# Kernel tuning notes

Hardware: AMD Instinct MI355X
Metric: run time of the kernel (lower is better)

## Reference

```python
import jax, jax.numpy as jnp
import numpy as np

K_PROPOSALS = 16  # Marsaglia-Tsang acceptance rate > 0.95 for alpha > 1/3; P(all 16 rejected) < 1e-20

B, D_IN, H, L = 32768, 1024, 512, 64


def _glorot(key, shape):
    fan_in, fan_out = shape
    return jax.random.normal(key, shape, jnp.float32) * jnp.sqrt(2.0 / (fan_in + fan_out))


def setup_inputs() -> dict:
    key = jax.random.key(0)
    ks = jax.random.split(key, 4)
    return {
        "x": jax.random.normal(ks[0], (B, D_IN), jnp.float32),
        "W0": _glorot(ks[1], (D_IN, H)),
        "b0": jnp.zeros((H,), jnp.float32),
        "W1": _glorot(ks[2], (H, H)),
        "b1": jnp.zeros((H,), jnp.float32),
        "Wl": _glorot(ks[3], (H, L)),
        "bl": jnp.zeros((L,), jnp.float32),
    }


def _marsaglia_tsang_sample(alpha):
    """Vectorized Marsaglia-Tsang gamma(alpha, 1) rejection sampler.
    Draws K_PROPOSALS candidates per element and selects the first accepted one
    (equivalent to the original per-element while-loop, flattened for SIMD)."""
    d = alpha - 1.0 / 3.0                     # [B, L]
    c = 1.0 / jnp.sqrt(9.0 * d)               # [B, L]
    kz, ku = jax.random.split(jax.random.key(1))
    z = jax.random.normal(kz, (K_PROPOSALS,) + alpha.shape, alpha.dtype)   # [K, B, L]
    u = jax.random.uniform(ku, (K_PROPOSALS,) + alpha.shape, alpha.dtype,
                           minval=1e-7, maxval=1.0)                        # [K, B, L]
    v = (1.0 + c * z) ** 3                    # [K, B, L]
    pos = v > 0.0                             # equivalent to z > -1/c (= b1)
    safe_v = jnp.where(pos, v, 1.0)
    # accept iff z > b1 AND log(u) <= b2 (negation of the resampling condition)
    b2 = 0.5 * jnp.square(z) + d - d * safe_v + d * jnp.log(safe_v)
    accept = pos & (jnp.log(u) < b2)          # [K, B, L]
    first = jnp.argmax(accept, axis=0)        # index of first accepted proposal
    samples = d * safe_v                      # [K, B, L]
    return jnp.take_along_axis(samples, first[None], axis=0)[0]  # [B, L]


def reference(x, W0, b0, W1, b1, Wl, bl):
    # dense encoder: two ReLU hidden layers + linear latent head producing alpha
    h = jax.nn.relu(x @ W0 + b0)
    h = jax.nn.relu(h @ W1 + b1)
    # softplus + 0.5 keeps alpha > 1/3 so d > 0 (required by Marsaglia-Tsang)
    alpha = jax.nn.softplus(h @ Wl + bl) + 0.5
    sample = _marsaglia_tsang_sample(alpha)
    return alpha, sample
```

## Files before the change

kernel.cpp:

```cpp
#include <hip/hip_runtime.h>
#include <cstdint>
#include <cstddef>

typedef __attribute__((ext_vector_type(8))) short short8;
typedef __attribute__((ext_vector_type(4))) float floatx4;

constexpr int MDIM = 32768;
constexpr int DIN  = 1024;
constexpr int HDIM = 512;
constexpr int LDIM = 64;
constexpr uint32_t BL = (uint32_t)MDIM * (uint32_t)LDIM;

__host__ __device__ __forceinline__ void tf2x32(uint32_t k0, uint32_t k1,
                                                uint32_t x0, uint32_t x1,
                                                uint32_t& o0, uint32_t& o1) {
  const uint32_t k2 = k0 ^ k1 ^ 0x1BD11BDAu;
  x0 += k0; x1 += k1;
#define TFR(r) { x0 += x1; x1 = (x1 << (r)) | (x1 >> (32 - (r))); x1 ^= x0; }
  TFR(13) TFR(15) TFR(26) TFR(6)
  x0 += k1; x1 += k2 + 1u;
  TFR(17) TFR(29) TFR(16) TFR(24)
  x0 += k2; x1 += k0 + 2u;
  TFR(13) TFR(15) TFR(26) TFR(6)
  x0 += k0; x1 += k1 + 3u;
  TFR(17) TFR(29) TFR(16) TFR(24)
  x0 += k1; x1 += k2 + 4u;
  TFR(13) TFR(15) TFR(26) TFR(6)
  x0 += k2; x1 += k0 + 5u;
#undef TFR
  o0 = x0; o1 = x1;
}

__device__ __forceinline__ uint32_t tf_bits(uint32_t k0, uint32_t k1, uint32_t j) {
  uint32_t o0, o1;
  tf2x32(k0, k1, 0u, j, o0, o1);
  return o0 ^ o1;
}

__device__ __forceinline__ float b2f(unsigned short s) {
  return __uint_as_float((uint32_t)s << 16);
}
__device__ __forceinline__ unsigned short f2b(float f) {
  uint32_t u = __float_as_uint(f);
  u += 0x7fffu + ((u >> 16) & 1u);
  return (unsigned short)(u >> 16);
}
__device__ __forceinline__ void split3(float x, unsigned short& h,
                                       unsigned short& l, unsigned short& l2) {
  h = f2b(x);
  const float r = __fsub_rn(x, b2f(h));
  l = f2b(r);
  const float r2 = __fsub_rn(r, b2f(l));
  l2 = f2b(r2);
}

__device__ __forceinline__ float erfinv_f32(float x) {
  const float xx = __fmul_rn(x, x);
  float w = -log1pf(-xx);
  float p;
  if (w < 5.0f) {
    w = __fadd_rn(w, -2.5f);
    p = 2.81022636e-08f;
    p = __fadd_rn(__fmul_rn(p, w), 3.43273939e-07f);
    p = __fadd_rn(__fmul_rn(p, w), -3.5233877e-06f);
    p = __fadd_rn(__fmul_rn(p, w), -4.39150654e-06f);
    p = __fadd_rn(__fmul_rn(p, w), 0.00021858087f);
    p = __fadd_rn(__fmul_rn(p, w), -0.00125372503f);
    p = __fadd_rn(__fmul_rn(p, w), -0.00417768164f);
    p = __fadd_rn(__fmul_rn(p, w), 0.246640727f);
    p = __fadd_rn(__fmul_rn(p, w), 1.50140941f);
  } else {
    w = __fadd_rn(sqrtf(w), -3.0f);
    p = -0.000200214257f;
    p = __fadd_rn(__fmul_rn(p, w), 0.000100950558f);
    p = __fadd_rn(__fmul_rn(p, w), 0.00134934322f);
    p = __fadd_rn(__fmul_rn(p, w), -0.00367342844f);
    p = __fadd_rn(__fmul_rn(p, w), 0.00573950773f);
    p = __fadd_rn(__fmul_rn(p, w), -0.0076224613f);
    p = __fadd_rn(__fmul_rn(p, w), 0.00943887047f);
    p = __fadd_rn(__fmul_rn(p, w), 1.00167406f);
    p = __fadd_rn(__fmul_rn(p, w), 2.83297682f);
  }
  return __fmul_rn(p, x);
}

#define LO_N  (-0x1.fffffep-1f)
#define DIFF_N (2.0f)
#define SQRT2_F ((float)1.4142135623730951)
#define DIFF_U (0x1.fffffcp-1f)
#define MINV_U (1e-7f)
#define THIRD_F ((float)(1.0 / 3.0))

__device__ float gamma_sample(float alpha, uint32_t e,
                              uint32_t kz0, uint32_t kz1,
                              uint32_t ku0, uint32_t ku1) {
  const float d = __fsub_rn(alpha, THIRD_F);
  const float c = __fdiv_rn(1.0f, sqrtf(__fmul_rn(9.0f, d)));
  float samp0 = 0.0f;
#pragma unroll 1
  for (int k = 0; k < 16; ++k) {
    const uint32_t j = (uint32_t)k * BL + e;
    const uint32_t zb = tf_bits(kz0, kz1, j);
    const uint32_t ub = tf_bits(ku0, ku1, j);
    const float fz = __fsub_rn(__uint_as_float((zb >> 9) | 0x3f800000u), 1.0f);
    float un = __fadd_rn(__fmul_rn(fz, DIFF_N), LO_N);
    un = fmaxf(un, LO_N);
    const float z = __fmul_rn(SQRT2_F, erfinv_f32(un));
    const float fu = __fsub_rn(__uint_as_float((ub >> 9) | 0x3f800000u), 1.0f);
    float uu = __fadd_rn(__fmul_rn(fu, DIFF_U), MINV_U);
    uu = fmaxf(uu, MINV_U);
    const float t1 = __fadd_rn(1.0f, __fmul_rn(c, z));
    const float v = __fmul_rn(t1, __fmul_rn(t1, t1));
    const bool pos = (v > 0.0f);
    const float sv = pos ? v : 1.0f;
    const float b2 = __fadd_rn(
        __fsub_rn(__fadd_rn(__fmul_rn(0.5f, __fmul_rn(z, z)), d),
                  __fmul_rn(d, sv)),
        __fmul_rn(d, logf(sv)));
    const float lu = logf(uu);
    const float s = __fmul_rn(d, sv);
    if (k == 0) samp0 = s;
    if (pos && (lu < b2)) return s;
  }
  return samp0;
}

__global__ __launch_bounds__(256) void split_transpose(
    const float* __restrict__ W, unsigned short* __restrict__ D, int K, int N) {
  __shared__ unsigned short th[32][33], tl[32][33], tl2[32][33];
  const int t = threadIdx.x;
  const int nb = N / 32;
  const int k0 = (blockIdx.x / nb) * 32, n0 = (blockIdx.x % nb) * 32;
#pragma unroll
  for (int i = 0; i < 4; ++i) {
    const int e = i * 256 + t;
    const int kk = e >> 5, nn = e & 31;
    const float x = W[(size_t)(k0 + kk) * N + (n0 + nn)];
    split3(x, th[kk][nn], tl[kk][nn], tl2[kk][nn]);
  }
  __syncthreads();
  const size_t PL = (size_t)N * K;
#pragma unroll
  for (int i = 0; i < 4; ++i) {
    const int e = i * 256 + t;
    const int nn = e >> 5, kk = e & 31;
    const size_t o = (size_t)(n0 + nn) * K + (k0 + kk);
    D[o] = th[kk][nn];
    D[PL + o] = tl[kk][nn];
    D[2 * PL + o] = tl2[kk][nn];
  }
}

template <int K>
__global__ __launch_bounds__(256) void gemm_split_mfma(
    const float* __restrict__ A, const unsigned short* __restrict__ BT,
    const float* __restrict__ bias, float* __restrict__ C) {
  constexpr int N = 512;
  constexpr size_t PL = (size_t)N * K;
  __shared__ unsigned short As[3][128 * 32];
  __shared__ unsigned short Bs[3][128 * 32];
  const int t = threadIdx.x;
  const int lane = t & 63, w = t >> 6;
  const int wm = w >> 1, wn = w & 1;
  const int ln = lane & 15, kq = lane >> 4;
  const int bid = blockIdx.y * gridDim.x + blockIdx.x;
  const int L = (bid & 7) * 128 + (bid >> 3);
  const int bm = (L >> 2) * 128, bn = (L & 3) * 128;
  const int rq = kq ^ ((ln >> 1) & 3);
  const int kcs = ((lane & 3) ^ ((lane >> 3) & 3)) * 8;

  floatx4 acc[4][4];
#pragma unroll
  for (int i = 0; i < 4; ++i)
#pragma unroll
    for (int j = 0; j < 4; ++j) acc[i][j] = (floatx4)0.0f;

  for (int k0 = 0; k0 < K; k0 += 32) {
#pragma unroll
    for (int p = 0; p < 3; ++p)
#pragma unroll
      for (int i = 0; i < 2; ++i) {
        const int e = w * 1024 + i * 512 + lane * 8;
        const int n = e >> 5;
        const unsigned short* g = BT + p * PL + (size_t)(bn + n) * K + (k0 + kcs);
        __builtin_amdgcn_global_load_lds(
            (const __attribute__((address_space(1))) unsigned int*)g,
            (__attribute__((address_space(3))) unsigned int*)&Bs[p][w * 1024 + i * 512],
            16, 0, 0);
      }
#pragma unroll
    for (int it = 0; it < 4; ++it) {
      const int e4 = (it * 256 + t) * 4;
      const int m = e4 >> 5, kc = e4 & 31;
      const float4 q = *reinterpret_cast<const float4*>(
          &A[(size_t)(bm + m) * K + (k0 + kc)]);
      ushort4 h, l, l2;
      split3(q.x, h.x, l.x, l2.x);
      split3(q.y, h.y, l.y, l2.y);
      split3(q.z, h.z, l.z, l2.z);
      split3(q.w, h.w, l.w, l2.w);
      const int si = m * 32 + (((kc >> 3) ^ ((m >> 1) & 3)) << 3) + (kc & 7);
      *reinterpret_cast<ushort4*>(&As[0][si]) = h;
      *reinterpret_cast<ushort4*>(&As[1][si]) = l;
      *reinterpret_cast<ushort4*>(&As[2][si]) = l2;
    }
    __syncthreads();
    short8 af[3][4], bf[3][4];
#pragma unroll
    for (int mi = 0; mi < 4; ++mi)
#pragma unroll
      for (int p = 0; p < 3; ++p)
        af[p][mi] = *reinterpret_cast<const short8*>(
            &As[p][(wm * 64 + mi * 16 + ln) * 32 + rq * 8]);
#pragma unroll
    for (int ni = 0; ni < 4; ++ni)
#pragma unroll
      for (int p = 0; p < 3; ++p)
        bf[p][ni] = *reinterpret_cast<const short8*>(
            &Bs[p][(wn * 64 + ni * 16 + ln) * 32 + rq * 8]);
#pragma unroll
    for (int mi = 0; mi < 4; ++mi)
#pragma unroll
      for (int ni = 0; ni < 4; ++ni) {
        floatx4 a = acc[mi][ni];
        a = __builtin_amdgcn_mfma_f32_16x16x32_bf16(af[0][mi], bf[0][ni], a, 0, 0, 0);
        a = __builtin_amdgcn_mfma_f32_16x16x32_bf16(af[0][mi], bf[1][ni], a, 0, 0, 0);
        a = __builtin_amdgcn_mfma_f32_16x16x32_bf16(af[1][mi], bf[0][ni], a, 0, 0, 0);
        a = __builtin_amdgcn_mfma_f32_16x16x32_bf16(af[1][mi], bf[1][ni], a, 0, 0, 0);
        a = __builtin_amdgcn_mfma_f32_16x16x32_bf16(af[0][mi], bf[2][ni], a, 0, 0, 0);
        a = __builtin_amdgcn_mfma_f32_16x16x32_bf16(af[2][mi], bf[0][ni], a, 0, 0, 0);
        acc[mi][ni] = a;
      }
    __syncthreads();
  }
#pragma unroll
  for (int ni = 0; ni < 4; ++ni) {
    const int n = bn + wn * 64 + ni * 16 + ln;
    const float bb = bias[n];
#pragma unroll
    for (int mi = 0; mi < 4; ++mi)
#pragma unroll
      for (int r = 0; r < 4; ++r) {
        const int m = bm + wm * 64 + mi * 16 + kq * 4 + r;
        C[(size_t)m * N + n] = fmaxf(__fadd_rn(acc[mi][ni][r], bb), 0.0f);
      }
  }
}

__global__ __launch_bounds__(256) void gemm3_alpha(
    const float* __restrict__ A, const unsigned short* __restrict__ BT,
    const float* __restrict__ bl, float* __restrict__ out) {
  constexpr int K = 512, N = 64;
  constexpr size_t PL = (size_t)N * K;
  __shared__ unsigned short As[3][64 * 32];
  __shared__ unsigned short Bs[3][64 * 32];
  const int t = threadIdx.x;
  const int lane = t & 63, w = t >> 6;
  const int ln = lane & 15, kq = lane >> 4;
  const int bm = blockIdx.x * 64;
  const int rq = kq ^ ((ln >> 1) & 3);
  const int kcs = ((lane & 3) ^ ((lane >> 3) & 3)) * 8;

  floatx4 acc[4];
#pragma unroll
  for (int j = 0; j < 4; ++j) acc[j] = (floatx4)0.0f;

  for (int k0 = 0; k0 < K; k0 += 32) {
#pragma unroll
    for (int p = 0; p < 3; ++p) {
      const int n = w * 16 + (lane >> 2);
      const unsigned short* g = BT + p * PL + (size_t)n * K + (k0 + kcs);
      __builtin_amdgcn_global_load_lds(
          (const __attribute__((address_space(1))) unsigned int*)g,
          (__attribute__((address_space(3))) unsigned int*)&Bs[p][w * 512],
          16, 0, 0);
    }
#pragma unroll
    for (int it = 0; it < 2; ++it) {
      const int e4 = (it * 256 + t) * 4;
      const int m = e4 >> 5, kc = e4 & 31;
      const float4 q = *reinterpret_cast<const float4*>(
          &A[(size_t)(bm + m) * K + (k0 + kc)]);
      ushort4 h, l, l2;
      split3(q.x, h.x, l.x, l2.x);
      split3(q.y, h.y, l.y, l2.y);
      split3(q.z, h.z, l.z, l2.z);
      split3(q.w, h.w, l.w, l2.w);
      const int si = m * 32 + (((kc >> 3) ^ ((m >> 1) & 3)) << 3) + (kc & 7);
      *reinterpret_cast<ushort4*>(&As[0][si]) = h;
      *reinterpret_cast<ushort4*>(&As[1][si]) = l;
      *reinterpret_cast<ushort4*>(&As[2][si]) = l2;
    }
    __syncthreads();
    short8 af[3];
#pragma unroll
    for (int p = 0; p < 3; ++p)
      af[p] = *reinterpret_cast<const short8*>(
          &As[p][(w * 16 + ln) * 32 + rq * 8]);
#pragma unroll
    for (int ni = 0; ni < 4; ++ni) {
      const short8 b0 = *reinterpret_cast<const short8*>(
          &Bs[0][(ni * 16 + ln) * 32 + rq * 8]);
      const short8 b1 = *reinterpret_cast<const short8*>(
          &Bs[1][(ni * 16 + ln) * 32 + rq * 8]);
      const short8 b2 = *reinterpret_cast<const short8*>(
          &Bs[2][(ni * 16 + ln) * 32 + rq * 8]);
      floatx4 a = acc[ni];
      a = __builtin_amdgcn_mfma_f32_16x16x32_bf16(af[0], b0, a, 0, 0, 0);
      a = __builtin_amdgcn_mfma_f32_16x16x32_bf16(af[0], b1, a, 0, 0, 0);
      a = __builtin_amdgcn_mfma_f32_16x16x32_bf16(af[1], b0, a, 0, 0, 0);
      a = __builtin_amdgcn_mfma_f32_16x16x32_bf16(af[1], b1, a, 0, 0, 0);
      a = __builtin_amdgcn_mfma_f32_16x16x32_bf16(af[0], b2, a, 0, 0, 0);
      a = __builtin_amdgcn_mfma_f32_16x16x32_bf16(af[2], b0, a, 0, 0, 0);
      acc[ni] = a;
    }
    __syncthreads();
  }
#pragma unroll
  for (int ni = 0; ni < 4; ++ni) {
    const int n = ni * 16 + ln;
    const float bb = bl[n];
#pragma unroll
    for (int r = 0; r < 4; ++r) {
      const int m = bm + w * 16 + kq * 4 + r;
      const float x = __fadd_rn(acc[ni][r], bb);
      const float sp = __fadd_rn(fmaxf(x, 0.0f), log1pf(expf(-fabsf(x))));
      out[(size_t)m * 64 + n] = __fadd_rn(sp, 0.5f);
    }
  }
}

__global__ __launch_bounds__(256) void gamma_kernel(
    const float* __restrict__ alpha, float* __restrict__ smp,
    uint32_t kz0, uint32_t kz1, uint32_t ku0, uint32_t ku1) {
  const uint32_t i4 = ((uint32_t)blockIdx.x * 256u + (uint32_t)threadIdx.x) * 4u;
  const float4 a = *reinterpret_cast<const float4*>(&alpha[i4]);
  float4 s;
  s.x = gamma_sample(a.x, i4 + 0u, kz0, kz1, ku0, ku1);
  s.y = gamma_sample(a.y, i4 + 1u, kz0, kz1, ku0, ku1);
  s.z = gamma_sample(a.z, i4 + 2u, kz0, kz1, ku0, ku1);
  s.w = gamma_sample(a.w, i4 + 3u, kz0, kz1, ku0, ku1);
  *reinterpret_cast<float4*>(&smp[i4]) = s;
}

extern "C" void kernel_launch(void* const* d_in, const int* in_sizes, int n_in,
                              void* d_out, int out_size, void* d_ws, size_t ws_size,
                              hipStream_t stream) {
  (void)in_sizes; (void)n_in; (void)out_size; (void)ws_size;
  const float* x  = (const float*)d_in[0];
  const float* W0 = (const float*)d_in[1];
  const float* b0 = (const float*)d_in[2];
  const float* W1 = (const float*)d_in[3];
  const float* b1 = (const float*)d_in[4];
  const float* Wl = (const float*)d_in[5];
  const float* bl = (const float*)d_in[6];
  float* h1 = (float*)d_ws;
  float* h2 = h1 + (size_t)MDIM * HDIM;
  float* out = (float*)d_out;

  unsigned short* W0T = (unsigned short*)out;
  unsigned short* W1T = (unsigned short*)(out + BL);
  unsigned short* WlT = (unsigned short*)d_ws;

  uint32_t kz0, kz1, ku0, ku1;
  tf2x32(0u, 1u, 0u, 0u, kz0, kz1);
  tf2x32(0u, 1u, 0u, 1u, ku0, ku1);

  split_transpose<<<dim3((DIN / 32) * (HDIM / 32)), 256, 0, stream>>>(
      W0, W0T, DIN, HDIM);
  split_transpose<<<dim3((HDIM / 32) * (HDIM / 32)), 256, 0, stream>>>(
      W1, W1T, HDIM, HDIM);

  dim3 g12(HDIM / 128, MDIM / 128);
  gemm_split_mfma<DIN><<<g12, 256, 0, stream>>>(x, W0T, b0, h1);
  gemm_split_mfma<HDIM><<<g12, 256, 0, stream>>>(h1, W1T, b1, h2);

  split_transpose<<<dim3((HDIM / 32) * (LDIM / 32)), 256, 0, stream>>>(
      Wl, WlT, HDIM, LDIM);

  gemm3_alpha<<<dim3(MDIM / 64), 256, 0, stream>>>(h2, WlT, bl, out);

  gamma_kernel<<<dim3(BL / 1024), 256, 0, stream>>>(out, out + BL,
                                                    kz0, kz1, ku0, ku1);
}
```

Measured before the change: 516.0 us.

## Use 512-thread blocks with 256-row tiles for split-bf16 GEMMs

The two hidden-layer GEMMs move from 256-thread blocks with 128x128 tiles to 512-thread blocks with 256x128 tiles, so each B tile is reused across twice as many rows. The swizzled block-ID remapping is dropped. The alpha GEMM also runs with 512 threads, using a 2D warp split so each wave handles 16 rows by 32 columns. The aim is less B-operand traffic per output and more waves per block. The costs are a larger LDS footprint, tighter register limits from launch_bounds(512,4), and the loss of the L2-friendly block ordering.

```diff
diff --git a/kernel.cpp b/kernel.cpp
--- a/kernel.cpp
+++ b/kernel.cpp
@@ -152,20 +152,18 @@
 }
 
 template <int K>
-__global__ __launch_bounds__(256) void gemm_split_mfma(
+__device__ __forceinline__ void gemm_body(
     const float* __restrict__ A, const unsigned short* __restrict__ BT,
     const float* __restrict__ bias, float* __restrict__ C) {
   constexpr int N = 512;
   constexpr size_t PL = (size_t)N * K;
-  __shared__ unsigned short As[3][128 * 32];
+  __shared__ unsigned short As[3][256 * 32];
   __shared__ unsigned short Bs[3][128 * 32];
   const int t = threadIdx.x;
   const int lane = t & 63, w = t >> 6;
   const int wm = w >> 1, wn = w & 1;
   const int ln = lane & 15, kq = lane >> 4;
-  const int bid = blockIdx.y * gridDim.x + blockIdx.x;
-  const int L = (bid & 7) * 128 + (bid >> 3);
-  const int bm = (L >> 2) * 128, bn = (L & 3) * 128;
+  const int bm = blockIdx.y * 256, bn = blockIdx.x * 128;
   const int rq = kq ^ ((ln >> 1) & 3);
   const int kcs = ((lane & 3) ^ ((lane >> 3) & 3)) * 8;
 
@@ -177,20 +175,17 @@
 
   for (int k0 = 0; k0 < K; k0 += 32) {
 #pragma unroll
-    for (int p = 0; p < 3; ++p)
-#pragma unroll
-      for (int i = 0; i < 2; ++i) {
-        const int e = w * 1024 + i * 512 + lane * 8;
-        const int n = e >> 5;
-        const unsigned short* g = BT + p * PL + (size_t)(bn + n) * K + (k0 + kcs);
-        __builtin_amdgcn_global_load_lds(
-            (const __attribute__((address_space(1))) unsigned int*)g,
-            (__attribute__((address_space(3))) unsigned int*)&Bs[p][w * 1024 + i * 512],
-            16, 0, 0);
-      }
+    for (int p = 0; p < 3; ++p) {
+      const int n = w * 16 + (lane >> 2);
+      const unsigned short* g = BT + p * PL + (size_t)(bn + n) * K + (k0 + kcs);
+      __builtin_amdgcn_global_load_lds(
+          (const __attribute__((address_space(1))) unsigned int*)g,
+          (__attribute__((address_space(3))) unsigned int*)&Bs[p][w * 512],
+          16, 0, 0);
+    }
 #pragma unroll
     for (int it = 0; it < 4; ++it) {
-      const int e4 = (it * 256 + t) * 4;
+      const int e4 = (it * 512 + t) * 4;
       const int m = e4 >> 5, kc = e4 & 31;
       const float4 q = *reinterpret_cast<const float4*>(
           &A[(size_t)(bm + m) * K + (k0 + kc)]);
@@ -247,7 +242,18 @@
   }
 }
 
-__global__ __launch_bounds__(256) void gemm3_alpha(
+__global__ __launch_bounds__(512, 4) void gemm1_k1024(
+    const float* __restrict__ A, const unsigned short* __restrict__ BT,
+    const float* __restrict__ bias, float* __restrict__ C) {
+  gemm_body<DIN>(A, BT, bias, C);
+}
+__global__ __launch_bounds__(512, 4) void gemm2_k512(
+    const float* __restrict__ A, const unsigned short* __restrict__ BT,
+    const float* __restrict__ bias, float* __restrict__ C) {
+  gemm_body<HDIM>(A, BT, bias, C);
+}
+
+__global__ __launch_bounds__(512, 4) void gemm3_alpha(
     const float* __restrict__ A, const unsigned short* __restrict__ BT,
     const float* __restrict__ bl, float* __restrict__ out) {
   constexpr int K = 512, N = 64;
@@ -256,74 +262,74 @@
   __shared__ unsigned short Bs[3][64 * 32];
   const int t = threadIdx.x;
   const int lane = t & 63, w = t >> 6;
+  const int wm = w >> 1, wn = w & 1;
   const int ln = lane & 15, kq = lane >> 4;
   const int bm = blockIdx.x * 64;
   const int rq = kq ^ ((ln >> 1) & 3);
   const int kcs = ((lane & 3) ^ ((lane >> 3) & 3)) * 8;
-
-  floatx4 acc[4];
-#pragma unroll
-  for (int j = 0; j < 4; ++j) acc[j] = (floatx4)0.0f;
+  const int arow = t >> 3, acol = (t * 4) & 31;
+  const int swz = ((((acol >> 3) ^ ((arow >> 1) & 3)) << 3) | (acol & 7));
+
+  floatx4 acc[2];
+  acc[0] = (floatx4)0.0f;
+  acc[1] = (floatx4)0.0f;
 
   for (int k0 = 0; k0 < K; k0 += 32) {
-#pragma unroll
-    for (int p = 0; p < 3; ++p) {
-      const int n = w * 16 + (lane >> 2);
+    for (int s2 = w; s2 < 12; s2 += 8) {
+      const int p = s2 >> 2, half = s2 & 3;
+      const int n = half * 16 + (lane >> 2);
       const unsigned short* g = BT + p * PL + (size_t)n * K + (k0 + kcs);
       __builtin_amdgcn_global_load_lds(
           (const __attribute__((address_space(1))) unsigned int*)g,
-          (__attribute__((address_space(3))) unsigned int*)&Bs[p][w * 512],
+          (__attribute__((address_space(3))) unsigned int*)&Bs[p][half * 512],
           16, 0, 0);
     }
-#pragma unroll
-    for (int it = 0; it < 2; ++it) {
-      const int e4 = (it * 256 + t) * 4;
-      const int m = e4 >> 5, kc = e4 & 31;
+    {
       const float4 q = *reinterpret_cast<const float4*>(
-          &A[(size_t)(bm + m) * K + (k0 + kc)]);
+          &A[(size_t)(bm + arow) * K + (k0 + acol)]);
       ushort4 h, l, l2;
       split3(q.x, h.x, l.x, l2.x);
       split3(q.y, h.y, l.y, l2.y);
       split3(q.z, h.z, l.z, l2.z);
       split3(q.w, h.w, l.w, l2.w);
-      const int si = m * 32 + (((kc >> 3) ^ ((m >> 1) & 3)) << 3) + (kc & 7);
+      const int si = arow * 32 + swz;
       *reinterpret_cast<ushort4*>(&As[0][si]) = h;
       *reinterpret_cast<ushort4*>(&As[1][si]) = l;
       *reinterpret_cast<ushort4*>(&As[2][si]) = l2;
     }
     __syncthreads();
-    short8 af[3];
+    short8 af[3], bf[3][2];
 #pragma unroll
     for (int p = 0; p < 3; ++p)
       af[p] = *reinterpret_cast<const short8*>(
-          &As[p][(w * 16 + ln) * 32 + rq * 8]);
-#pragma unroll
-    for (int ni = 0; ni < 4; ++ni) {
-      const short8 b0 = *reinterpret_cast<const short8*>(
-          &Bs[0][(ni * 16 + ln) * 32 + rq * 8]);
-      const short8 b1 = *reinterpret_cast<const short8*>(
-          &Bs[1][(ni * 16 + ln) * 32 + rq * 8]);
-      const short8 b2 = *reinterpret_cast<const short8*>(
-          &Bs[2][(ni * 16 + ln) * 32 + rq * 8]);
-      floatx4 a = acc[ni];
-      a = __builtin_amdgcn_mfma_f32_16x16x32_bf16(af[0], b0, a, 0, 0, 0);
-      a = __builtin_amdgcn_mfma_f32_16x16x32_bf16(af[0], b1, a, 0, 0, 0);
-      a = __builtin_amdgcn_mfma_f32_16x16x32_bf16(af[1], b0, a, 0, 0, 0);
-      a = __builtin_amdgcn_mfma_f32_16x16x32_bf16(af[1], b1, a, 0, 0, 0);
-      a = __builtin_amdgcn_mfma_f32_16x16x32_bf16(af[0], b2, a, 0, 0, 0);
-      a = __builtin_amdgcn_mfma_f32_16x16x32_bf16(af[2], b0, a, 0, 0, 0);
-      acc[ni] = a;
+          &As[p][(wm * 16 + ln) * 32 + rq * 8]);
+#pragma unroll
+    for (int j = 0; j < 2; ++j)
+#pragma unroll
+      for (int p = 0; p < 3; ++p)
+        bf[p][j] = *reinterpret_cast<const short8*>(
+            &Bs[p][(wn * 32 + j * 16 + ln) * 32 + rq * 8]);
+#pragma unroll
+    for (int j = 0; j < 2; ++j) {
+      floatx4 a = acc[j];
+      a = __builtin_amdgcn_mfma_f32_16x16x32_bf16(af[0], bf[0][j], a, 0, 0, 0);
+      a = __builtin_amdgcn_mfma_f32_16x16x32_bf16(af[0], bf[1][j], a, 0, 0, 0);
+      a = __builtin_amdgcn_mfma_f32_16x16x32_bf16(af[1], bf[0][j], a, 0, 0, 0);
+      a = __builtin_amdgcn_mfma_f32_16x16x32_bf16(af[1], bf[1][j], a, 0, 0, 0);
+      a = __builtin_amdgcn_mfma_f32_16x16x32_bf16(af[0], bf[2][j], a, 0, 0, 0);
+      a = __builtin_amdgcn_mfma_f32_16x16x32_bf16(af[2], bf[0][j], a, 0, 0, 0);
+      acc[j] = a;
     }
     __syncthreads();
   }
 #pragma unroll
-  for (int ni = 0; ni < 4; ++ni) {
-    const int n = ni * 16 + ln;
+  for (int j = 0; j < 2; ++j) {
+    const int n = wn * 32 + j * 16 + ln;
     const float bb = bl[n];
 #pragma unroll
     for (int r = 0; r < 4; ++r) {
-      const int m = bm + w * 16 + kq * 4 + r;
-      const float x = __fadd_rn(acc[ni][r], bb);
+      const int m = bm + wm * 16 + kq * 4 + r;
+      const float x = __fadd_rn(acc[j][r], bb);
       const float sp = __fadd_rn(fmaxf(x, 0.0f), log1pf(expf(-fabsf(x))));
       out[(size_t)m * 64 + n] = __fadd_rn(sp, 0.5f);
     }
@@ -371,14 +377,14 @@
   split_transpose<<<dim3((HDIM / 32) * (HDIM / 32)), 256, 0, stream>>>(
       W1, W1T, HDIM, HDIM);
 
-  dim3 g12(HDIM / 128, MDIM / 128);
-  gemm_split_mfma<DIN><<<g12, 256, 0, stream>>>(x, W0T, b0, h1);
-  gemm_split_mfma<HDIM><<<g12, 256, 0, stream>>>(h1, W1T, b1, h2);
+  dim3 g12(HDIM / 128, MDIM / 256);
+  gemm1_k1024<<<g12, 512, 0, stream>>>(x, W0T, b0, h1);
+  gemm2_k512<<<g12, 512, 0, stream>>>(h1, W1T, b1, h2);
 
   split_transpose<<<dim3((HDIM / 32) * (LDIM / 32)), 256, 0, stream>>>(
       Wl, WlT, HDIM, LDIM);
 
-  gemm3_alpha<<<dim3(MDIM / 64), 256, 0, stream>>>(h2, WlT, bl, out);
+  gemm3_alpha<<<dim3(MDIM / 64), 512, 0, stream>>>(h2, WlT, bl, out);
 
   gamma_kernel<<<dim3(BL / 1024), 256, 0, stream>>>(out, out + BL,
                                                     kz0, kz1, ku0, ku1);
```

Result: slower. 538.6 us (+4.4%).

## Switch split-bf16 GEMMs to 32x32x16 MFMA and split first GEMM launch

Applied to the files above, without the earlier changes.

Replaces the 16x16x32 bf16 MFMA tiling in the two hidden-layer GEMMs with 32x32x16 MFMA, using 2x2 floatx16 accumulators per wave. Each k-step is split into two 16-wide sub-steps with matching swizzled LDS reads. The goal is fewer LDS fragment loads per FLOP and higher MFMA throughput. It also drops the block-index remapping swizzle and launches the first GEMM as two half-M kernels, which may change L2 locality and adds a launch.

```diff
diff --git a/kernel.cpp b/kernel.cpp
--- a/kernel.cpp
+++ b/kernel.cpp
@@ -4,6 +4,7 @@
 
 typedef __attribute__((ext_vector_type(8))) short short8;
 typedef __attribute__((ext_vector_type(4))) float floatx4;
+typedef __attribute__((ext_vector_type(16))) float floatx16;
 
 constexpr int MDIM = 32768;
 constexpr int DIN  = 1024;
@@ -152,9 +153,9 @@
 }
 
 template <int K>
-__global__ __launch_bounds__(256) void gemm_split_mfma(
+__device__ __forceinline__ void gemm_body32(
     const float* __restrict__ A, const unsigned short* __restrict__ BT,
-    const float* __restrict__ bias, float* __restrict__ C) {
+    const float* __restrict__ bias, float* __restrict__ C, const int bm) {
   constexpr int N = 512;
   constexpr size_t PL = (size_t)N * K;
   __shared__ unsigned short As[3][128 * 32];
@@ -162,18 +163,17 @@
   const int t = threadIdx.x;
   const int lane = t & 63, w = t >> 6;
   const int wm = w >> 1, wn = w & 1;
-  const int ln = lane & 15, kq = lane >> 4;
-  const int bid = blockIdx.y * gridDim.x + blockIdx.x;
-  const int L = (bid & 7) * 128 + (bid >> 3);
-  const int bm = (L >> 2) * 128, bn = (L & 3) * 128;
-  const int rq = kq ^ ((ln >> 1) & 3);
+  const int l31 = lane & 31, l5 = lane >> 5;
+  const int bn = blockIdx.x * 128;
   const int kcs = ((lane & 3) ^ ((lane >> 3) & 3)) * 8;
 
-  floatx4 acc[4][4];
-#pragma unroll
-  for (int i = 0; i < 4; ++i)
-#pragma unroll
-    for (int j = 0; j < 4; ++j) acc[i][j] = (floatx4)0.0f;
+  floatx16 acc[2][2];
+#pragma unroll
+  for (int i = 0; i < 2; ++i)
+#pragma unroll
+    for (int j = 0; j < 2; ++j)
+#pragma unroll
+      for (int q = 0; q < 16; ++q) acc[i][j][q] = 0.0f;
 
   for (int k0 = 0; k0 < K; k0 += 32) {
 #pragma unroll
@@ -205,46 +205,70 @@
       *reinterpret_cast<ushort4*>(&As[2][si]) = l2;
     }
     __syncthreads();
-    short8 af[3][4], bf[3][4];
-#pragma unroll
-    for (int mi = 0; mi < 4; ++mi)
-#pragma unroll
-      for (int p = 0; p < 3; ++p)
-        af[p][mi] = *reinterpret_cast<const short8*>(
-            &As[p][(wm * 64 + mi * 16 + ln) * 32 + rq * 8]);
-#pragma unroll
-    for (int ni = 0; ni < 4; ++ni)
-#pragma unroll
-      for (int p = 0; p < 3; ++p)
-        bf[p][ni] = *reinterpret_cast<const short8*>(
-            &Bs[p][(wn * 64 + ni * 16 + ln) * 32 + rq * 8]);
-#pragma unroll
-    for (int mi = 0; mi < 4; ++mi)
-#pragma unroll
-      for (int ni = 0; ni < 4; ++ni) {
-        floatx4 a = acc[mi][ni];
-        a = __builtin_amdgcn_mfma_f32_16x16x32_bf16(af[0][mi], bf[0][ni], a, 0, 0, 0);
-        a = __builtin_amdgcn_mfma_f32_16x16x32_bf16(af[0][mi], bf[1][ni], a, 0, 0, 0);
-        a = __builtin_amdgcn_mfma_f32_16x16x32_bf16(af[1][mi], bf[0][ni], a, 0, 0, 0);
-        a = __builtin_amdgcn_mfma_f32_16x16x32_bf16(af[1][mi], bf[1][ni], a, 0, 0, 0);
-        a = __builtin_amdgcn_mfma_f32_16x16x32_bf16(af[0][mi], bf[2][ni], a, 0, 0, 0);
-        a = __builtin_amdgcn_mfma_f32_16x16x32_bf16(af[2][mi], bf[0][ni], a, 0, 0, 0);
-        acc[mi][ni] = a;
+#pragma unroll
+    for (int ks = 0; ks < 2; ++ks) {
+      const int g = ks * 2 + l5;
+      short8 af[3][2], bf[3][2];
+#pragma unroll
+      for (int mi = 0; mi < 2; ++mi)
+#pragma unroll
+        for (int p = 0; p < 3; ++p) {
+          const int row = wm * 64 + mi * 32 + l31;
+          af[p][mi] = *reinterpret_cast<const short8*>(
+              &As[p][row * 32 + ((g ^ ((row >> 1) & 3)) << 3)]);
+        }
+#pragma unroll
+      for (int ni = 0; ni < 2; ++ni)
+#pragma unroll
+        for (int p = 0; p < 3; ++p) {
+          const int row = wn * 64 + ni * 32 + l31;
+          bf[p][ni] = *reinterpret_cast<const short8*>(
+              &Bs[p][row * 32 + ((g ^ ((row >> 1) & 3)) << 3)]);
+        }
+#pragma unroll
+      for (int mi = 0; mi < 2; ++mi)
+#pragma unroll
+        for (int ni = 0; ni < 2; ++ni) {
+          floatx16 a = acc[mi][ni];
+          a = __builtin_amdgcn_mfma_f32_32x32x16_bf16(af[0][mi], bf[0][ni], a, 0, 0, 0);
+          a = __builtin_amdgcn_mfma_f32_32x32x16_bf16(af[0][mi], bf[1][ni], a, 0, 0, 0);
+          a = __builtin_amdgcn_mfma_f32_32x32x16_bf16(af[1][mi], bf[0][ni], a, 0, 0, 0);
+          a = __builtin_amdgcn_mfma_f32_32x32x16_bf16(af[1][mi], bf[1][ni], a, 0, 0, 0);
+          a = __builtin_amdgcn_mfma_f32_32x32x16_bf16(af[0][mi], bf[2][ni], a, 0, 0, 0);
+          a = __builtin_amdgcn_mfma_f32_32x32x16_bf16(af[2][mi], bf[0][ni], a, 0, 0, 0);
+          acc[mi][ni] = a;
+        }
+    }
+    __syncthreads();
+  }
+#pragma unroll
+  for (int ni = 0; ni < 2; ++ni) {
+    const int col = bn + wn * 64 + ni * 32 + l31;
+    const float bb = bias[col];
+#pragma unroll
+    for (int mi = 0; mi < 2; ++mi)
+#pragma unroll
+      for (int r = 0; r < 16; ++r) {
+        const int row = bm + wm * 64 + mi * 32 + (r & 3) + 8 * (r >> 2) + 4 * l5;
+        C[(size_t)row * N + col] = fmaxf(__fadd_rn(acc[mi][ni][r], bb), 0.0f);
       }
-    __syncthreads();
-  }
-#pragma unroll
-  for (int ni = 0; ni < 4; ++ni) {
-    const int n = bn + wn * 64 + ni * 16 + ln;
-    const float bb = bias[n];
-#pragma unroll
-    for (int mi = 0; mi < 4; ++mi)
-#pragma unroll
-      for (int r = 0; r < 4; ++r) {
-        const int m = bm + wm * 64 + mi * 16 + kq * 4 + r;
-        C[(size_t)m * N + n] = fmaxf(__fadd_rn(acc[mi][ni][r], bb), 0.0f);
-      }
-  }
+  }
+}
+
+__global__ __launch_bounds__(256) void gemm1a(
+    const float* __restrict__ A, const unsigned short* __restrict__ BT,
+    const float* __restrict__ bias, float* __restrict__ C) {
+  gemm_body32<DIN>(A, BT, bias, C, blockIdx.y * 128);
+}
+__global__ __launch_bounds__(256) void gemm1b(
+    const float* __restrict__ A, const unsigned short* __restrict__ BT,
+    const float* __restrict__ bias, float* __restrict__ C) {
+  gemm_body32<DIN>(A, BT, bias, C, MDIM / 2 + blockIdx.y * 128);
+}
+__global__ __launch_bounds__(256) void gemm2_k512(
+    const float* __restrict__ A, const unsigned short* __restrict__ BT,
+    const float* __restrict__ bias, float* __restrict__ C) {
+  gemm_body32<HDIM>(A, BT, bias, C, blockIdx.y * 128);
 }
 
 __global__ __launch_bounds__(256) void gemm3_alpha(
@@ -371,9 +395,9 @@
   split_transpose<<<dim3((HDIM / 32) * (HDIM / 32)), 256, 0, stream>>>(
       W1, W1T, HDIM, HDIM);
 
-  dim3 g12(HDIM / 128, MDIM / 128);
-  gemm_split_mfma<DIN><<<g12, 256, 0, stream>>>(x, W0T, b0, h1);
-  gemm_split_mfma<HDIM><<<g12, 256, 0, stream>>>(h1, W1T, b1, h2);
+  gemm1a<<<dim3(HDIM / 128, MDIM / 256), 256, 0, stream>>>(x, W0T, b0, h1);
+  gemm1b<<<dim3(HDIM / 128, MDIM / 256), 256, 0, stream>>>(x, W0T, b0, h1);
+  gemm2_k512<<<dim3(HDIM / 128, MDIM / 128), 256, 0, stream>>>(h1, W1T, b1, h2);
 
   split_transpose<<<dim3((HDIM / 32) * (LDIM / 32)), 256, 0, stream>>>(
       Wl, WlT, HDIM, LDIM);
```

After: 546.8 us. +6.0%, slower.

## Split GEMM launches into row chunks and use one element per gamma thread

Applied to the files above, without the earlier changes.

Splits the first two GEMMs into several smaller launches over row ranges (3 for layer 1, 2 for layer 2), each with a plain blockIdx.x column mapping in place of the swizzled tile ordering. The gamma kernel now processes one element per thread instead of four with float4 loads. The intent is probably to change wave scheduling and tail behaviour and to raise parallelism in the divergent sampler. In exchange it drops the L2-friendly tile swizzle, adds launch overhead and loses vectorized memory access.

```diff
diff --git a/kernel.cpp b/kernel.cpp
--- a/kernel.cpp
+++ b/kernel.cpp
@@ -152,9 +152,9 @@
 }
 
 template <int K>
-__global__ __launch_bounds__(256) void gemm_split_mfma(
-    const float* __restrict__ A, const unsigned short* __restrict__ BT,
-    const float* __restrict__ bias, float* __restrict__ C) {
+__device__ __forceinline__ void gemm_body16(
+    const float* __restrict__ A, const unsigned short* __restrict__ BT,
+    const float* __restrict__ bias, float* __restrict__ C, const int bm) {
   constexpr int N = 512;
   constexpr size_t PL = (size_t)N * K;
   __shared__ unsigned short As[3][128 * 32];
@@ -163,9 +163,7 @@
   const int lane = t & 63, w = t >> 6;
   const int wm = w >> 1, wn = w & 1;
   const int ln = lane & 15, kq = lane >> 4;
-  const int bid = blockIdx.y * gridDim.x + blockIdx.x;
-  const int L = (bid & 7) * 128 + (bid >> 3);
-  const int bm = (L >> 2) * 128, bn = (L & 3) * 128;
+  const int bn = blockIdx.x * 128;
   const int rq = kq ^ ((ln >> 1) & 3);
   const int kcs = ((lane & 3) ^ ((lane >> 3) & 3)) * 8;
 
@@ -247,6 +245,32 @@
   }
 }
 
+__global__ __launch_bounds__(256) void gemm1a(
+    const float* __restrict__ A, const unsigned short* __restrict__ BT,
+    const float* __restrict__ bias, float* __restrict__ C) {
+  gemm_body16<DIN>(A, BT, bias, C, blockIdx.y * 128);
+}
+__global__ __launch_bounds__(256) void gemm1b(
+    const float* __restrict__ A, const unsigned short* __restrict__ BT,
+    const float* __restrict__ bias, float* __restrict__ C) {
+  gemm_body16<DIN>(A, BT, bias, C, (86 + blockIdx.y) * 128);
+}
+__global__ __launch_bounds__(256) void gemm1c(
+    const float* __restrict__ A, const unsigned short* __restrict__ BT,
+    const float* __restrict__ bias, float* __restrict__ C) {
+  gemm_body16<DIN>(A, BT, bias, C, (171 + blockIdx.y) * 128);
+}
+__global__ __launch_bounds__(256) void gemm2a(
+    const float* __restrict__ A, const unsigned short* __restrict__ BT,
+    const float* __restrict__ bias, float* __restrict__ C) {
+  gemm_body16<HDIM>(A, BT, bias, C, blockIdx.y * 128);
+}
+__global__ __launch_bounds__(256) void gemm2b(
+    const float* __restrict__ A, const unsigned short* __restrict__ BT,
+    const float* __restrict__ bias, float* __restrict__ C) {
+  gemm_body16<HDIM>(A, BT, bias, C, (128 + blockIdx.y) * 128);
+}
+
 __global__ __launch_bounds__(256) void gemm3_alpha(
     const float* __restrict__ A, const unsigned short* __restrict__ BT,
     const float* __restrict__ bl, float* __restrict__ out) {
@@ -333,14 +357,8 @@
 __global__ __launch_bounds__(256) void gamma_kernel(
     const float* __restrict__ alpha, float* __restrict__ smp,
     uint32_t kz0, uint32_t kz1, uint32_t ku0, uint32_t ku1) {
-  const uint32_t i4 = ((uint32_t)blockIdx.x * 256u + (uint32_t)threadIdx.x) * 4u;
-  const float4 a = *reinterpret_cast<const float4*>(&alpha[i4]);
-  float4 s;
-  s.x = gamma_sample(a.x, i4 + 0u, kz0, kz1, ku0, ku1);
-  s.y = gamma_sample(a.y, i4 + 1u, kz0, kz1, ku0, ku1);
-  s.z = gamma_sample(a.z, i4 + 2u, kz0, kz1, ku0, ku1);
-  s.w = gamma_sample(a.w, i4 + 3u, kz0, kz1, ku0, ku1);
-  *reinterpret_cast<float4*>(&smp[i4]) = s;
+  const uint32_t i = (uint32_t)blockIdx.x * 256u + (uint32_t)threadIdx.x;
+  smp[i] = gamma_sample(alpha[i], i, kz0, kz1, ku0, ku1);
 }
 
 extern "C" void kernel_launch(void* const* d_in, const int* in_sizes, int n_in,
@@ -371,15 +389,17 @@
   split_transpose<<<dim3((HDIM / 32) * (HDIM / 32)), 256, 0, stream>>>(
       W1, W1T, HDIM, HDIM);
 
-  dim3 g12(HDIM / 128, MDIM / 128);
-  gemm_split_mfma<DIN><<<g12, 256, 0, stream>>>(x, W0T, b0, h1);
-  gemm_split_mfma<HDIM><<<g12, 256, 0, stream>>>(h1, W1T, b1, h2);
+  gemm1a<<<dim3(HDIM / 128, 86), 256, 0, stream>>>(x, W0T, b0, h1);
+  gemm1b<<<dim3(HDIM / 128, 85), 256, 0, stream>>>(x, W0T, b0, h1);
+  gemm1c<<<dim3(HDIM / 128, 85), 256, 0, stream>>>(x, W0T, b0, h1);
+  gemm2a<<<dim3(HDIM / 128, 128), 256, 0, stream>>>(h1, W1T, b1, h2);
+  gemm2b<<<dim3(HDIM / 128, 128), 256, 0, stream>>>(h1, W1T, b1, h2);
 
   split_transpose<<<dim3((HDIM / 32) * (LDIM / 32)), 256, 0, stream>>>(
       Wl, WlT, HDIM, LDIM);
 
   gemm3_alpha<<<dim3(MDIM / 64), 256, 0, stream>>>(h2, WlT, bl, out);
 
-  gamma_kernel<<<dim3(BL / 1024), 256, 0, stream>>>(out, out + BL,
-                                                    kz0, kz1, ku0, ku1);
-}
+  gamma_kernel<<<dim3(BL / 256), 256, 0, stream>>>(out, out + BL,
+                                                   kz0, kz1, ku0, ku1);
+}
```

New measurement: 568.6 us. 1.1x slower.
